# Kernel optimization log

Measured on AMD Instinct MI355X. Metric: run time of the kernel, lower is better.

The kernel has to match this reference:

```python
import jax, jax.numpy as jnp
import numpy as np

B, N, H_IN, H_HID, N_HEAD = 32, 500, 64, 16, 8
N_VALID = 400  # valid (non-padded) nodes per graph; node 0 is the root
NEG_INF = -1e20


def setup_inputs() -> dict:
    key = jax.random.key(0)
    ks = jax.random.split(key, 10)
    x = jax.random.normal(ks[0], (B, N, H_IN), jnp.float32)
    # sparse-ish binary adjacency with self loops
    A = (jax.random.uniform(ks[1], (B, N, N)) < 0.05).astype(jnp.float32)
    A = jnp.maximum(A, jnp.eye(N, dtype=jnp.float32)[None])
    # mask_nonzero: first N_VALID nodes of every graph are valid
    mask_batch = jnp.repeat(jnp.arange(B, dtype=jnp.int32), N_VALID)
    mask_row = jnp.tile(jnp.arange(N_VALID, dtype=jnp.int32), B)
    s = 0.1
    w1 = jax.random.normal(ks[2], (N_HEAD, H_IN, H_HID), jnp.float32) * s
    a_src1 = jax.random.normal(ks[3], (N_HEAD, H_HID), jnp.float32) * s
    a_dst1 = jax.random.normal(ks[4], (N_HEAD, H_HID), jnp.float32) * s
    w2 = jax.random.normal(ks[5], (1, N_HEAD * H_HID, H_IN), jnp.float32) * s
    a_src2 = jax.random.normal(ks[6], (1, H_IN), jnp.float32) * s
    a_dst2 = jax.random.normal(ks[7], (1, H_IN), jnp.float32) * s
    attn_w = jax.random.normal(ks[8], (2 * H_IN,), jnp.float32) * s
    return {"x": x, "A": A, "mask_batch": mask_batch, "mask_row": mask_row,
            "w1": w1, "a_src1": a_src1, "a_dst1": a_dst1,
            "w2": w2, "a_src2": a_src2, "a_dst2": a_dst2, "attn_w": attn_w}


def gat_layer(h_in, A, w, a_src, a_dst):
    # h_in: [B,N,F_in]; w: [H,F_in,F_out]
    h = jnp.einsum('bnf,hfo->bhno', h_in, w)              # [B,H,N,F_out]
    e_src = jnp.einsum('bhno,ho->bhn', h, a_src)          # [B,H,N]
    e_dst = jnp.einsum('bhno,ho->bhn', h, a_dst)
    e = jax.nn.leaky_relu(e_src[..., :, None] + e_dst[..., None, :], 0.2)  # [B,H,N,N]
    e = jnp.where(A[:, None, :, :] > 0, e, NEG_INF)
    attn = jax.nn.softmax(e, axis=-1)
    return jnp.einsum('bhnm,bhmo->bhno', attn, h)         # [B,H,N,F_out]


def reference(x, A, mask_batch, mask_row, w1, a_src1, a_dst1, w2, a_src2, a_dst2, attn_w):
    b, n, _ = x.shape
    # BatchGAT encoder: layer 1 (multi-head, concat + ELU), layer 2 (1 head -> h_in)
    h1 = gat_layer(x, A, w1, a_src1, a_dst1)                       # [B,H,N,h_hid]
    h1 = jax.nn.elu(h1).transpose(0, 2, 1, 3).reshape(b, n, -1)    # [B,N,H*h_hid]
    xc = gat_layer(h1, A, w2, a_src2, a_dst2)[:, 0]                # [B,N,h_in]
    # zero out padded nodes (so their Post_Attn scores are exactly 0)
    valid = jnp.zeros((b, n), x.dtype).at[mask_batch, mask_row].set(1.0)
    xc = xc * valid[:, :, None]
    # Post_Attn: scatter root features to each valid node position
    root = jnp.zeros_like(xc).at[mask_batch, mask_row, :].set(xc[mask_batch, 0, :])
    x_plus = jnp.concatenate([xc, root], axis=-1)                  # [B,N,2*h_in]
    score = x_plus @ attn_w                                        # [B,N]
    score = jnp.where(score == 0, NEG_INF, score)[:, :, None]      # masked_fill
    attn = jax.nn.softmax(score, axis=1)                           # softmax over nodes
    pooled = jnp.einsum('bnf,bn->bf', xc, attn[:, :, 0])           # [B,h_in]
    return pooled, attn
```

## Files before the change

kernel.cpp:

```cpp
#include <hip/hip_runtime.h>

#define NB 32
#define NN 500
#define HIN 64
#define HHID 16
#define NHEAD 8
#define NVALID 400
#define MAXK 128
#define NEG_INF -1e20f

__global__ __launch_bounds__(256) void k_pre(const float* __restrict__ A,
                                             int* __restrict__ nbr, int* __restrict__ cnt,
                                             const float* __restrict__ x, const float* __restrict__ w1,
                                             const float* __restrict__ as1, const float* __restrict__ ad1,
                                             float* __restrict__ h1p, float* __restrict__ e1s,
                                             float* __restrict__ e1d)
{
    int bid = blockIdx.x;
    if (bid < 4000) {
        int row = bid * 4 + (threadIdx.x >> 6);
        int lane = threadIdx.x & 63;
        const float4* arow4 = (const float4*)(A + (size_t)row * NN);
        int* np = nbr + (size_t)row * MAXK;
        int c = 0;
#pragma unroll
        for (int it = 0; it < 2; ++it) {
            int idx = it * 64 + lane;
            float4 av;
            if (idx < 125) av = arow4[idx];
            else { av.x = av.y = av.z = av.w = 0.f; }
            bool v0 = av.x > 0.f, v1 = av.y > 0.f, v2 = av.z > 0.f, v3 = av.w > 0.f;
            unsigned long long b0 = __ballot(v0), b1 = __ballot(v1);
            unsigned long long b2 = __ballot(v2), b3 = __ballot(v3);
            unsigned long long below = (1ull << lane) - 1ull;
            int p = c + __popcll(b0 & below) + __popcll(b1 & below)
                      + __popcll(b2 & below) + __popcll(b3 & below);
            int col = idx * 4;
            if (v0 && p < MAXK) np[p] = col;     p += (int)v0;
            if (v1 && p < MAXK) np[p] = col + 1; p += (int)v1;
            if (v2 && p < MAXK) np[p] = col + 2; p += (int)v2;
            if (v3 && p < MAXK) np[p] = col + 3; p += (int)v3;
            c += (int)(__popcll(b0) + __popcll(b1) + __popcll(b2) + __popcll(b3));
        }
        if (lane == 0) cnt[row] = c < MAXK ? c : MAXK;
        return;
    }
    int pb = bid - 4000;
    int b = pb >> 5, chunk = pb & 31;
    int t = threadIdx.x, slot = t >> 7, lane = t & 127;
    int h = lane >> 4, o = lane & 15;
    float wreg[64];
#pragma unroll
    for (int f = 0; f < 64; ++f) wreg[f] = w1[h * 1024 + f * 16 + o];
    float as_r = as1[h * 16 + o], ad_r = ad1[h * 16 + o];
    __shared__ __align__(16) float xs[2][64];
    for (int i = 0; i < 8; ++i) {
        int n = chunk * 16 + i * 2 + slot;
        bool valid = n < NN;
        if (valid && lane < 64) xs[slot][lane] = x[(size_t)(b * NN + n) * HIN + lane];
        __syncthreads();
        if (valid) {
            float acc = 0.f;
#pragma unroll
            for (int f4 = 0; f4 < 16; ++f4) {
                float4 xv = *(const float4*)&xs[slot][f4 * 4];
                acc += xv.x * wreg[f4 * 4] + xv.y * wreg[f4 * 4 + 1]
                     + xv.z * wreg[f4 * 4 + 2] + xv.w * wreg[f4 * 4 + 3];
            }
            h1p[(size_t)(b * NN + n) * 128 + lane] = acc;
            float vs = acc * as_r, vd = acc * ad_r;
#pragma unroll
            for (int m = 1; m < 16; m <<= 1) { vs += __shfl_xor(vs, m); vd += __shfl_xor(vd, m); }
            if (o == 0) {
                e1s[(size_t)(b * NN + n) * 8 + h] = vs;
                e1d[(size_t)(b * NN + n) * 8 + h] = vd;
            }
        }
        __syncthreads();
    }
}

__global__ __launch_bounds__(128) void k_agg1(const int* __restrict__ nbr, const int* __restrict__ cnt,
                                              const float* __restrict__ h1p, const float* __restrict__ e1s,
                                              const float* __restrict__ e1d, float* __restrict__ h1cat)
{
    int bid = blockIdx.x;
    int xcd = bid & 7, g = bid >> 3;
    int b = (g / NN) * 8 + xcd;
    int n = g % NN;
    int row = b * NN + n;
    int t = threadIdx.x;
    int h = t >> 4, o = t & 15;
    __shared__ int nb_s[MAXK];
    __shared__ float p_s[NHEAD][MAXK + 4];
    int K = cnt[row];
    for (int k = t; k < K; k += 128) nb_s[k] = nbr[(size_t)row * MAXK + k];
    __syncthreads();
    float es = e1s[(size_t)row * 8 + h];
    float r[8];
    float mx = -1e30f;
#pragma unroll
    for (int j = 0; j < 8; ++j) {
        int k = o + j * 16;
        if (k < K) {
            float e = es + e1d[(size_t)(b * NN + nb_s[k]) * 8 + h];
            e = e > 0.f ? e : 0.2f * e;
            r[j] = e;
            mx = fmaxf(mx, e);
        }
    }
#pragma unroll
    for (int m = 1; m < 16; m <<= 1) mx = fmaxf(mx, __shfl_xor(mx, m));
    float sum = 0.f;
#pragma unroll
    for (int j = 0; j < 8; ++j) {
        int k = o + j * 16;
        if (k < K) { float v = __expf(r[j] - mx); r[j] = v; sum += v; }
    }
#pragma unroll
    for (int m = 1; m < 16; m <<= 1) sum += __shfl_xor(sum, m);
    float inv = 1.f / sum;
#pragma unroll
    for (int j = 0; j < 8; ++j) {
        int k = o + j * 16;
        if (k < K) p_s[h][k] = r[j] * inv;
    }
    __syncthreads();
    float acc = 0.f;
    const float* hp = h1p + (size_t)b * NN * 128 + t;
    int k = 0;
    for (; k + 4 <= K; k += 4) {
        float a0 = hp[(size_t)nb_s[k] * 128];
        float a1 = hp[(size_t)nb_s[k + 1] * 128];
        float a2 = hp[(size_t)nb_s[k + 2] * 128];
        float a3 = hp[(size_t)nb_s[k + 3] * 128];
        acc += p_s[h][k] * a0;
        acc += p_s[h][k + 1] * a1;
        acc += p_s[h][k + 2] * a2;
        acc += p_s[h][k + 3] * a3;
    }
    for (; k < K; ++k) acc += p_s[h][k] * hp[(size_t)nb_s[k] * 128];
    h1cat[(size_t)row * 128 + t] = acc > 0.f ? acc : expm1f(acc);
}

__global__ __launch_bounds__(256) void k_proj2(const float* __restrict__ h1cat, const float* __restrict__ w2,
                                               const float* __restrict__ as2, const float* __restrict__ ad2,
                                               float* __restrict__ h2p, float* __restrict__ e2s,
                                               float* __restrict__ e2d)
{
    int b = blockIdx.y, chunk = blockIdx.x;
    int t = threadIdx.x, slot = t >> 7, lane = t & 127;
    int fh = lane >> 6, o = lane & 63;
    float wreg[64];
#pragma unroll
    for (int j = 0; j < 64; ++j) wreg[j] = w2[(fh * 64 + j) * 64 + o];
    float as_r = as2[o], ad_r = ad2[o];
    __shared__ __align__(16) float xs[2][128];
    __shared__ float part[2][128];
    for (int i = 0; i < 8; ++i) {
        int n = chunk * 16 + i * 2 + slot;
        bool valid = n < NN;
        if (valid) xs[slot][lane] = h1cat[(size_t)(b * NN + n) * 128 + lane];
        __syncthreads();
        float acc = 0.f;
        if (valid) {
#pragma unroll
            for (int j4 = 0; j4 < 16; ++j4) {
                float4 xv = *(const float4*)&xs[slot][fh * 64 + j4 * 4];
                acc += xv.x * wreg[j4 * 4] + xv.y * wreg[j4 * 4 + 1]
                     + xv.z * wreg[j4 * 4 + 2] + xv.w * wreg[j4 * 4 + 3];
            }
        }
        part[slot][lane] = acc;
        __syncthreads();
        if (valid && fh == 0) {
            float val = acc + part[slot][64 + o];
            h2p[(size_t)(b * NN + n) * 64 + o] = val;
            float vs = val * as_r, vd = val * ad_r;
#pragma unroll
            for (int m = 1; m < 64; m <<= 1) { vs += __shfl_xor(vs, m); vd += __shfl_xor(vd, m); }
            if (o == 0) { e2s[b * NN + n] = vs; e2d[b * NN + n] = vd; }
        }
        __syncthreads();
    }
}

__global__ __launch_bounds__(64) void k_agg2(const int* __restrict__ nbr, const int* __restrict__ cnt,
                                             const float* __restrict__ h2p, const float* __restrict__ e2s,
                                             const float* __restrict__ e2d, const float* __restrict__ aw,
                                             float* __restrict__ xc, float* __restrict__ sc,
                                             float* __restrict__ root_dot)
{
    int bid = blockIdx.x;
    int xcd = bid & 7, g = bid >> 3;
    int b = (g / NN) * 8 + xcd;
    int n = g % NN;
    int row = b * NN + n;
    int t = threadIdx.x;
    if (n >= NVALID) { xc[(size_t)row * 64 + t] = 0.f; return; }
    __shared__ int nb_s[MAXK];
    __shared__ float p_s[MAXK];
    int K = cnt[row];
    for (int k = t; k < K; k += 64) nb_s[k] = nbr[(size_t)row * MAXK + k];
    __syncthreads();
    float es = e2s[row];
    float r0 = -1e30f, r1 = -1e30f;
    if (t < K) {
        float e = es + e2d[b * NN + nb_s[t]];
        r0 = e > 0.f ? e : 0.2f * e;
    }
    if (t + 64 < K) {
        float e = es + e2d[b * NN + nb_s[t + 64]];
        r1 = e > 0.f ? e : 0.2f * e;
    }
    float mx = fmaxf(r0, r1);
#pragma unroll
    for (int m = 1; m < 64; m <<= 1) mx = fmaxf(mx, __shfl_xor(mx, m));
    float v0 = (t < K) ? __expf(r0 - mx) : 0.f;
    float v1 = (t + 64 < K) ? __expf(r1 - mx) : 0.f;
    float sum = v0 + v1;
#pragma unroll
    for (int m = 1; m < 64; m <<= 1) sum += __shfl_xor(sum, m);
    float inv = 1.f / sum;
    if (t < K) p_s[t] = v0 * inv;
    if (t + 64 < K) p_s[t + 64] = v1 * inv;
    __syncthreads();
    float acc = 0.f;
    const float* h2b = h2p + (size_t)b * NN * 64 + t;
    int k = 0;
    for (; k + 4 <= K; k += 4) {
        float a0 = h2b[(size_t)nb_s[k] * 64];
        float a1 = h2b[(size_t)nb_s[k + 1] * 64];
        float a2 = h2b[(size_t)nb_s[k + 2] * 64];
        float a3 = h2b[(size_t)nb_s[k + 3] * 64];
        acc += p_s[k] * a0;
        acc += p_s[k + 1] * a1;
        acc += p_s[k + 2] * a2;
        acc += p_s[k + 3] * a3;
    }
    for (; k < K; ++k) acc += p_s[k] * h2b[(size_t)nb_s[k] * 64];
    xc[(size_t)row * 64 + t] = acc;
    float v = acc * aw[t];
#pragma unroll
    for (int m = 1; m < 64; m <<= 1) v += __shfl_xor(v, m);
    if (t == 0) sc[row] = v;
    if (n == 0) {
        float v2 = acc * aw[64 + t];
#pragma unroll
        for (int m = 1; m < 64; m <<= 1) v2 += __shfl_xor(v2, m);
        if (t == 0) root_dot[b] = v2;
    }
}

__global__ __launch_bounds__(1024) void k_pool(const float* __restrict__ xc, const float* __restrict__ sc,
                                               const float* __restrict__ root_dot, float* __restrict__ out)
{
    int b = blockIdx.x;
    int t = threadIdx.x, w = t >> 6, lane = t & 63;
    __shared__ float attn_s[NN];
    __shared__ float red[16];
    __shared__ float part[16][64];
    const float* xb = xc + (size_t)b * NN * 64;
    float rd = root_dot[b];
    float s = NEG_INF;
    if (t < NVALID) {
        s = sc[b * NN + t] + rd;
        if (s == 0.f) s = NEG_INF;
    }
    float mx = s;
#pragma unroll
    for (int m = 1; m < 64; m <<= 1) mx = fmaxf(mx, __shfl_xor(mx, m));
    if (lane == 0) red[w] = mx;
    __syncthreads();
    mx = red[0];
#pragma unroll
    for (int i = 1; i < 16; ++i) mx = fmaxf(mx, red[i]);
    float e = (t < NN) ? __expf(s - mx) : 0.f;
    float sum = e;
#pragma unroll
    for (int m = 1; m < 64; m <<= 1) sum += __shfl_xor(sum, m);
    __syncthreads();
    if (lane == 0) red[w] = sum;
    __syncthreads();
    sum = 0.f;
#pragma unroll
    for (int i = 0; i < 16; ++i) sum += red[i];
    float inv = 1.f / sum;
    if (t < NN) {
        float a = e * inv;
        out[NB * 64 + b * NN + t] = a;
        attn_s[t] = a;
    }
    __syncthreads();
    float acc = 0.f;
    for (int n = w; n < NN; n += 16) acc += attn_s[n] * xb[(size_t)n * 64 + lane];
    part[w][lane] = acc;
    __syncthreads();
    if (t < 64) {
        float v = 0.f;
#pragma unroll
        for (int i = 0; i < 16; ++i) v += part[i][t];
        out[b * 64 + t] = v;
    }
}

extern "C" void kernel_launch(void* const* d_in, const int* in_sizes, int n_in,
                              void* d_out, int out_size, void* d_ws, size_t ws_size,
                              hipStream_t stream) {
    const float* x   = (const float*)d_in[0];
    const float* A   = (const float*)d_in[1];
    const float* w1  = (const float*)d_in[4];
    const float* as1 = (const float*)d_in[5];
    const float* ad1 = (const float*)d_in[6];
    const float* w2  = (const float*)d_in[7];
    const float* as2 = (const float*)d_in[8];
    const float* ad2 = (const float*)d_in[9];
    const float* aw  = (const float*)d_in[10];
    float* out = (float*)d_out;

    char* ws = (char*)d_ws;
    int* nbr = (int*)ws;
    int* cnt = (int*)(ws + (size_t)16000 * 128 * 4);
    float* f = (float*)(ws + (size_t)16000 * 129 * 4);
    float* h1p   = f;  f += (size_t)NB * NN * 128;
    float* e1s   = f;  f += (size_t)NB * NN * NHEAD;
    float* e1d   = f;  f += (size_t)NB * NN * NHEAD;
    float* h1cat = f;  f += (size_t)NB * NN * 128;
    float* h2p   = f;  f += (size_t)NB * NN * 64;
    float* e2s   = f;  f += (size_t)NB * NN;
    float* e2d   = f;  f += (size_t)NB * NN;
    float* xc    = f;  f += (size_t)NB * NN * 64;
    float* sc    = f;  f += (size_t)NB * NN;
    float* rootd = f;  f += NB;

    hipLaunchKernelGGL(k_pre,   dim3(5024),   dim3(256), 0, stream, A, nbr, cnt, x, w1, as1, ad1, h1p, e1s, e1d);
    hipLaunchKernelGGL(k_agg1,  dim3(NB * NN), dim3(128), 0, stream, nbr, cnt, h1p, e1s, e1d, h1cat);
    hipLaunchKernelGGL(k_proj2, dim3(32, NB), dim3(256), 0, stream, h1cat, w2, as2, ad2, h2p, e2s, e2d);
    hipLaunchKernelGGL(k_agg2,  dim3(NB * NN), dim3(64), 0, stream, nbr, cnt, h2p, e2s, e2d, aw, xc, sc, rootd);
    hipLaunchKernelGGL(k_pool,  dim3(NB),     dim3(1024), 0, stream, xc, sc, rootd, out);
}
```

Baseline: 163.5 us.

## Fuse layer-2 projection into layer-1 aggregation and batch x loads in k_pre

Merges the second GAT layer's projection (h1cat @ w2 plus attention logits) into the per-node layer-1 aggregation kernel. This removes one launch and the h1cat round trip through global memory. k_pre now loads all 16 node rows of x into shared memory at once instead of syncing twice per iteration. The gather loops in both aggregation kernels are unrolled to 8 loads for more memory parallelism, and k_agg2 keeps neighbor indices in registers. The cost is that every block now reads w2 from global or cache directly rather than holding it in registers, so each node re-reads 32 KB of weights.

```diff
diff --git a/kernel.cpp b/kernel.cpp
--- a/kernel.cpp
+++ b/kernel.cpp
@@ -53,17 +53,22 @@
 #pragma unroll
     for (int f = 0; f < 64; ++f) wreg[f] = w1[h * 1024 + f * 16 + o];
     float as_r = as1[h * 16 + o], ad_r = ad1[h * 16 + o];
-    __shared__ __align__(16) float xs[2][64];
+    __shared__ __align__(16) float xs[16][64];
+    {
+        int node = chunk * 16 + (t >> 4);
+        float4 v = make_float4(0.f, 0.f, 0.f, 0.f);
+        if (node < NN) v = *(const float4*)&x[(size_t)(b * NN + node) * HIN + ((t * 4) & 63)];
+        *(float4*)&xs[t >> 4][(t * 4) & 63] = v;
+    }
+    __syncthreads();
     for (int i = 0; i < 8; ++i) {
         int n = chunk * 16 + i * 2 + slot;
-        bool valid = n < NN;
-        if (valid && lane < 64) xs[slot][lane] = x[(size_t)(b * NN + n) * HIN + lane];
-        __syncthreads();
-        if (valid) {
+        if (n < NN) {
+            const float* xrow = xs[i * 2 + slot];
             float acc = 0.f;
 #pragma unroll
             for (int f4 = 0; f4 < 16; ++f4) {
-                float4 xv = *(const float4*)&xs[slot][f4 * 4];
+                float4 xv = *(const float4*)&xrow[f4 * 4];
                 acc += xv.x * wreg[f4 * 4] + xv.y * wreg[f4 * 4 + 1]
                      + xv.z * wreg[f4 * 4 + 2] + xv.w * wreg[f4 * 4 + 3];
             }
@@ -76,13 +81,15 @@
                 e1d[(size_t)(b * NN + n) * 8 + h] = vd;
             }
         }
-        __syncthreads();
-    }
-}
-
-__global__ __launch_bounds__(128) void k_agg1(const int* __restrict__ nbr, const int* __restrict__ cnt,
-                                              const float* __restrict__ h1p, const float* __restrict__ e1s,
-                                              const float* __restrict__ e1d, float* __restrict__ h1cat)
+    }
+}
+
+__global__ __launch_bounds__(128) void k_agg1p2(const int* __restrict__ nbr, const int* __restrict__ cnt,
+                                                const float* __restrict__ h1p, const float* __restrict__ e1s,
+                                                const float* __restrict__ e1d, const float* __restrict__ w2,
+                                                const float* __restrict__ as2, const float* __restrict__ ad2,
+                                                float* __restrict__ h2p, float* __restrict__ e2s,
+                                                float* __restrict__ e2d)
 {
     int bid = blockIdx.x;
     int xcd = bid & 7, g = bid >> 3;
@@ -91,8 +98,11 @@
     int row = b * NN + n;
     int t = threadIdx.x;
     int h = t >> 4, o = t & 15;
+    int half = t >> 6, o2 = t & 63;
     __shared__ int nb_s[MAXK];
     __shared__ float p_s[NHEAD][MAXK + 4];
+    __shared__ __align__(16) float hc[128];
+    __shared__ float part[128];
     int K = cnt[row];
     for (int k = t; k < K; k += 128) nb_s[k] = nbr[(size_t)row * MAXK + k];
     __syncthreads();
@@ -129,59 +139,44 @@
     float acc = 0.f;
     const float* hp = h1p + (size_t)b * NN * 128 + t;
     int k = 0;
-    for (; k + 4 <= K; k += 4) {
+    for (; k + 8 <= K; k += 8) {
         float a0 = hp[(size_t)nb_s[k] * 128];
         float a1 = hp[(size_t)nb_s[k + 1] * 128];
         float a2 = hp[(size_t)nb_s[k + 2] * 128];
         float a3 = hp[(size_t)nb_s[k + 3] * 128];
+        float a4 = hp[(size_t)nb_s[k + 4] * 128];
+        float a5 = hp[(size_t)nb_s[k + 5] * 128];
+        float a6 = hp[(size_t)nb_s[k + 6] * 128];
+        float a7 = hp[(size_t)nb_s[k + 7] * 128];
         acc += p_s[h][k] * a0;
         acc += p_s[h][k + 1] * a1;
         acc += p_s[h][k + 2] * a2;
         acc += p_s[h][k + 3] * a3;
+        acc += p_s[h][k + 4] * a4;
+        acc += p_s[h][k + 5] * a5;
+        acc += p_s[h][k + 6] * a6;
+        acc += p_s[h][k + 7] * a7;
     }
     for (; k < K; ++k) acc += p_s[h][k] * hp[(size_t)nb_s[k] * 128];
-    h1cat[(size_t)row * 128 + t] = acc > 0.f ? acc : expm1f(acc);
-}
-
-__global__ __launch_bounds__(256) void k_proj2(const float* __restrict__ h1cat, const float* __restrict__ w2,
-                                               const float* __restrict__ as2, const float* __restrict__ ad2,
-                                               float* __restrict__ h2p, float* __restrict__ e2s,
-                                               float* __restrict__ e2d)
-{
-    int b = blockIdx.y, chunk = blockIdx.x;
-    int t = threadIdx.x, slot = t >> 7, lane = t & 127;
-    int fh = lane >> 6, o = lane & 63;
-    float wreg[64];
-#pragma unroll
-    for (int j = 0; j < 64; ++j) wreg[j] = w2[(fh * 64 + j) * 64 + o];
-    float as_r = as2[o], ad_r = ad2[o];
-    __shared__ __align__(16) float xs[2][128];
-    __shared__ float part[2][128];
-    for (int i = 0; i < 8; ++i) {
-        int n = chunk * 16 + i * 2 + slot;
-        bool valid = n < NN;
-        if (valid) xs[slot][lane] = h1cat[(size_t)(b * NN + n) * 128 + lane];
-        __syncthreads();
-        float acc = 0.f;
-        if (valid) {
-#pragma unroll
-            for (int j4 = 0; j4 < 16; ++j4) {
-                float4 xv = *(const float4*)&xs[slot][fh * 64 + j4 * 4];
-                acc += xv.x * wreg[j4 * 4] + xv.y * wreg[j4 * 4 + 1]
-                     + xv.z * wreg[j4 * 4 + 2] + xv.w * wreg[j4 * 4 + 3];
-            }
-        }
-        part[slot][lane] = acc;
-        __syncthreads();
-        if (valid && fh == 0) {
-            float val = acc + part[slot][64 + o];
-            h2p[(size_t)(b * NN + n) * 64 + o] = val;
-            float vs = val * as_r, vd = val * ad_r;
-#pragma unroll
-            for (int m = 1; m < 64; m <<= 1) { vs += __shfl_xor(vs, m); vd += __shfl_xor(vd, m); }
-            if (o == 0) { e2s[b * NN + n] = vs; e2d[b * NN + n] = vd; }
-        }
-        __syncthreads();
+    hc[t] = acc > 0.f ? acc : expm1f(acc);
+    __syncthreads();
+    const float* wbase = w2 + (size_t)(half * 64) * 64 + o2;
+    float acc2 = 0.f;
+#pragma unroll
+    for (int j4 = 0; j4 < 16; ++j4) {
+        float4 hv = *(const float4*)&hc[half * 64 + j4 * 4];
+        acc2 += hv.x * wbase[(j4 * 4 + 0) * 64] + hv.y * wbase[(j4 * 4 + 1) * 64]
+              + hv.z * wbase[(j4 * 4 + 2) * 64] + hv.w * wbase[(j4 * 4 + 3) * 64];
+    }
+    part[t] = acc2;
+    __syncthreads();
+    if (half == 0) {
+        float val = acc2 + part[64 + o2];
+        h2p[(size_t)row * 64 + o2] = val;
+        float vs = val * as2[o2], vd = val * ad2[o2];
+#pragma unroll
+        for (int m = 1; m < 64; m <<= 1) { vs += __shfl_xor(vs, m); vd += __shfl_xor(vd, m); }
+        if (o2 == 0) { e2s[row] = vs; e2d[row] = vd; }
     }
 }
 
@@ -201,16 +196,18 @@
     __shared__ int nb_s[MAXK];
     __shared__ float p_s[MAXK];
     int K = cnt[row];
-    for (int k = t; k < K; k += 64) nb_s[k] = nbr[(size_t)row * MAXK + k];
+    int nb0 = 0, nb1 = 0;
+    if (t < K)      { nb0 = nbr[(size_t)row * MAXK + t];      nb_s[t] = nb0; }
+    if (t + 64 < K) { nb1 = nbr[(size_t)row * MAXK + t + 64]; nb_s[t + 64] = nb1; }
     __syncthreads();
     float es = e2s[row];
     float r0 = -1e30f, r1 = -1e30f;
     if (t < K) {
-        float e = es + e2d[b * NN + nb_s[t]];
+        float e = es + e2d[b * NN + nb0];
         r0 = e > 0.f ? e : 0.2f * e;
     }
     if (t + 64 < K) {
-        float e = es + e2d[b * NN + nb_s[t + 64]];
+        float e = es + e2d[b * NN + nb1];
         r1 = e > 0.f ? e : 0.2f * e;
     }
     float mx = fmaxf(r0, r1);
@@ -228,15 +225,23 @@
     float acc = 0.f;
     const float* h2b = h2p + (size_t)b * NN * 64 + t;
     int k = 0;
-    for (; k + 4 <= K; k += 4) {
+    for (; k + 8 <= K; k += 8) {
         float a0 = h2b[(size_t)nb_s[k] * 64];
         float a1 = h2b[(size_t)nb_s[k + 1] * 64];
         float a2 = h2b[(size_t)nb_s[k + 2] * 64];
         float a3 = h2b[(size_t)nb_s[k + 3] * 64];
+        float a4 = h2b[(size_t)nb_s[k + 4] * 64];
+        float a5 = h2b[(size_t)nb_s[k + 5] * 64];
+        float a6 = h2b[(size_t)nb_s[k + 6] * 64];
+        float a7 = h2b[(size_t)nb_s[k + 7] * 64];
         acc += p_s[k] * a0;
         acc += p_s[k + 1] * a1;
         acc += p_s[k + 2] * a2;
         acc += p_s[k + 3] * a3;
+        acc += p_s[k + 4] * a4;
+        acc += p_s[k + 5] * a5;
+        acc += p_s[k + 6] * a6;
+        acc += p_s[k + 7] * a7;
     }
     for (; k < K; ++k) acc += p_s[k] * h2b[(size_t)nb_s[k] * 64];
     xc[(size_t)row * 64 + t] = acc;
@@ -325,7 +330,6 @@
     float* h1p   = f;  f += (size_t)NB * NN * 128;
     float* e1s   = f;  f += (size_t)NB * NN * NHEAD;
     float* e1d   = f;  f += (size_t)NB * NN * NHEAD;
-    float* h1cat = f;  f += (size_t)NB * NN * 128;
     float* h2p   = f;  f += (size_t)NB * NN * 64;
     float* e2s   = f;  f += (size_t)NB * NN;
     float* e2d   = f;  f += (size_t)NB * NN;
@@ -333,9 +337,8 @@
     float* sc    = f;  f += (size_t)NB * NN;
     float* rootd = f;  f += NB;
 
-    hipLaunchKernelGGL(k_pre,   dim3(5024),   dim3(256), 0, stream, A, nbr, cnt, x, w1, as1, ad1, h1p, e1s, e1d);
-    hipLaunchKernelGGL(k_agg1,  dim3(NB * NN), dim3(128), 0, stream, nbr, cnt, h1p, e1s, e1d, h1cat);
-    hipLaunchKernelGGL(k_proj2, dim3(32, NB), dim3(256), 0, stream, h1cat, w2, as2, ad2, h2p, e2s, e2d);
-    hipLaunchKernelGGL(k_agg2,  dim3(NB * NN), dim3(64), 0, stream, nbr, cnt, h2p, e2s, e2d, aw, xc, sc, rootd);
-    hipLaunchKernelGGL(k_pool,  dim3(NB),     dim3(1024), 0, stream, xc, sc, rootd, out);
-}
+    hipLaunchKernelGGL(k_pre,    dim3(5024),    dim3(256), 0, stream, A, nbr, cnt, x, w1, as1, ad1, h1p, e1s, e1d);
+    hipLaunchKernelGGL(k_agg1p2, dim3(NB * NN), dim3(128), 0, stream, nbr, cnt, h1p, e1s, e1d, w2, as2, ad2, h2p, e2s, e2d);
+    hipLaunchKernelGGL(k_agg2,   dim3(NB * NN), dim3(64),  0, stream, nbr, cnt, h2p, e2s, e2d, aw, xc, sc, rootd);
+    hipLaunchKernelGGL(k_pool,   dim3(NB),      dim3(1024), 0, stream, xc, sc, rootd, out);
+}
```

After: 159.8 us. 2.3% less time.
